# Kernel tuning notes

Measured on AMD Instinct MI355X. Metric: run time of the kernel, lower is better.

## Reference

```python
import jax, jax.numpy as jnp
import numpy as np

B, M, D, H = 32768, 4, 256, 8
HD = D // H           # head_dim = 32
DG = 64               # gate hidden (d_a)
DF = 4 * D            # FF hidden = 1024
EPS = 1e-5


def setup_inputs() -> dict:
    key = jax.random.key(0)
    ks = jax.random.split(key, 20)
    s = 0.02
    inp = {
        'x':   jax.random.normal(ks[0], (B, M, D), jnp.float32),
        # per-modality MultiheadAttention params (stacked over modality axis)
        'Wq':  jax.random.normal(ks[1], (M, D, D), jnp.float32) * s,
        'bq':  jnp.zeros((M, D), jnp.float32),
        'Wk':  jax.random.normal(ks[2], (M, D, D), jnp.float32) * s,
        'bk':  jnp.zeros((M, D), jnp.float32),
        'Wv':  jax.random.normal(ks[3], (M, D, D), jnp.float32) * s,
        'bv':  jnp.zeros((M, D), jnp.float32),
        'Wo':  jax.random.normal(ks[4], (M, D, D), jnp.float32) * s,
        'bo':  jnp.zeros((M, D), jnp.float32),
        # gate MLP: Linear(2D,64) -> tanh -> Linear(64,1)
        'g1w': jax.random.normal(ks[5], (M, DG, 2 * D), jnp.float32) * s,
        'g1b': jnp.zeros((M, DG), jnp.float32),
        'g2w': jax.random.normal(ks[6], (M, 1, DG), jnp.float32) * s,
        'g2b': jnp.zeros((M, 1), jnp.float32),
        # LayerNorm
        'ln_g': jnp.ones((M, D), jnp.float32),
        'ln_b': jnp.zeros((M, D), jnp.float32),
        # FeedForward: Linear(D,4D) -> GELU -> Linear(4D,D)
        'f1w': jax.random.normal(ks[7], (M, DF, D), jnp.float32) * s,
        'f1b': jnp.zeros((M, DF), jnp.float32),
        'f2w': jax.random.normal(ks[8], (M, D, DF), jnp.float32) * s,
        'f2b': jnp.zeros((M, D), jnp.float32),
    }
    return inp


def _forward(x, Wq, bq, Wk, bk, Wv, bv, Wo, bo, g1w, g1b, g2w, g2b,
             ln_g, ln_b, f1w, f1b, f2w, f2b):
    b = x.shape[0]
    scale = 1.0 / np.sqrt(HD)
    # cross-attention: per modality m, query = x[:,m] (seq 1), keys/values = all modalities (seq M)
    Q = jnp.einsum('bmd,mkd->bmk', x, Wq) + bq                      # [B,M,D]
    K = jnp.einsum('bnd,mkd->bmnk', x, Wk) + bk[None, :, None, :]   # [B,M,N,D]
    V = jnp.einsum('bnd,mkd->bmnk', x, Wv) + bv[None, :, None, :]
    Qh = Q.reshape(b, M, H, HD) * scale
    Kh = K.reshape(b, M, M, H, HD)
    Vh = V.reshape(b, M, M, H, HD)
    scores = jnp.einsum('bmhd,bmnhd->bmhn', Qh, Kh)                 # [B,M,H,N]
    A = jax.nn.softmax(scores, axis=-1)
    Oh = jnp.einsum('bmhn,bmnhd->bmhd', A, Vh).reshape(b, M, D)
    attn_out = jnp.einsum('bmd,mod->bmo', Oh, Wo) + bo              # [B,M,D]
    # gate: sigmoid(MLP([x; attn_out]))
    combined = jnp.concatenate([x, attn_out], axis=-1)              # [B,M,2D]
    h = jnp.tanh(jnp.einsum('bmd,mhd->bmh', combined, g1w) + g1b)
    gate = jax.nn.sigmoid(jnp.einsum('bmh,moh->bmo', h, g2w) + g2b) # [B,M,1]
    # residual + LayerNorm (per modality affine)
    r = x + gate * attn_out
    mu = jnp.mean(r, axis=-1, keepdims=True)
    var = jnp.mean(jnp.square(r - mu), axis=-1, keepdims=True)
    y = (r - mu) * jax.lax.rsqrt(var + EPS) * ln_g + ln_b
    # FeedForward residual (exact GELU, matching torch nn.GELU default)
    hf = jax.nn.gelu(jnp.einsum('bmd,mhd->bmh', y, f1w) + f1b, approximate=False)
    ff = jnp.einsum('bmh,mdh->bmd', hf, f2w) + f2b
    updated = y + ff
    return updated, gate


def reference(x, Wq, bq, Wk, bk, Wv, bv, Wo, bo, g1w, g1b, g2w, g2b,
              ln_g, ln_b, f1w, f1b, f2w, f2b):
    return _forward(x, Wq, bq, Wk, bk, Wv, bv, Wo, bo, g1w, g1b, g2w, g2b,
                    ln_g, ln_b, f1w, f1b, f2w, f2b)
```

## Files before the change

kernel.cpp:

```cpp
#include <hip/hip_runtime.h>

#define B_SZ 32768
#define M_SZ 4
#define D_SZ 256
#define SCALE_Q 0.17677669529663687f

#define OWQ 0
#define OWK 262144
#define OWV 524288
#define OWO 786432
#define OG1 1048576
#define OF1 1179648
#define OF2 2228224
#define NW_TOT 3276800

typedef __attribute__((ext_vector_type(8))) short bf16x8;
typedef __attribute__((ext_vector_type(4))) float f32x4;

__device__ __forceinline__ short f2b(float f){
  unsigned u = __float_as_uint(f);
  return (short)((u + 0x7FFFu + ((u >> 16) & 1u)) >> 16);
}
__device__ __forceinline__ float b2f(short s){
  return __uint_as_float(((unsigned)(unsigned short)s) << 16);
}
__device__ __forceinline__ float bflo(unsigned u){ return __uint_as_float(u << 16); }
__device__ __forceinline__ float bfhi(unsigned u){ return __uint_as_float(u & 0xFFFF0000u); }
__device__ __forceinline__ unsigned pack2(float a, float b){
  return (unsigned)(unsigned short)f2b(a) | (((unsigned)(unsigned short)f2b(b)) << 16);
}

__global__ void k_cast_w(const float* __restrict__ Wq, const float* __restrict__ Wk,
                         const float* __restrict__ Wv, const float* __restrict__ Wo,
                         const float* __restrict__ g1w, const float* __restrict__ f1w,
                         const float* __restrict__ f2w, short* __restrict__ wsW){
  int i = blockIdx.x * 256 + threadIdx.x;
  if (i >= NW_TOT) return;
  const float* src; int off;
  if (i < OG1){ int r = i >> 18; off = i & 262143;
    src = (r == 0) ? Wq : (r == 1) ? Wk : (r == 2) ? Wv : Wo; }
  else if (i < OF1){ src = g1w; off = i - OG1; }
  else if (i < OF2){ src = f1w; off = i - OF1; }
  else { src = f2w; off = i - OF2; }
  wsW[i] = f2b(src[off]);
}

__device__ __forceinline__ void kv_gemm(const short* __restrict__ wmat, const float* __restrict__ bias,
                                        const short* xb_s, short* kv_s, int w, int cl, int kb){
  f32x4 acc[4][2];
#pragma unroll
  for (int rt = 0; rt < 4; ++rt)
#pragma unroll
    for (int c = 0; c < 2; ++c) acc[rt][c] = (f32x4){0.f,0.f,0.f,0.f};
  for (int kk = 0; kk < 8; ++kk){
    bf16x8 a[4];
#pragma unroll
    for (int rt = 0; rt < 4; ++rt)
      a[rt] = *(const bf16x8*)&xb_s[(rt*16 + cl)*264 + kk*32 + kb*8];
#pragma unroll
    for (int c = 0; c < 2; ++c){
      int col = (2*w + c)*16 + cl;
      bf16x8 b = *(const bf16x8*)&wmat[(size_t)col*256 + kk*32 + kb*8];
#pragma unroll
      for (int rt = 0; rt < 4; ++rt)
        acc[rt][c] = __builtin_amdgcn_mfma_f32_16x16x32_bf16(a[rt], b, acc[rt][c], 0, 0, 0);
    }
  }
#pragma unroll
  for (int c = 0; c < 2; ++c){
    int col = (2*w + c)*16 + cl;
    float bs = bias[col];
#pragma unroll
    for (int rt = 0; rt < 4; ++rt)
#pragma unroll
      for (int i = 0; i < 4; ++i)
        kv_s[(rt*16 + kb*4 + i)*264 + col] = f2b(acc[rt][c][i] + bs);
  }
}

__global__ __launch_bounds__(512, 1)
void k_attn(const float* __restrict__ x, const short* __restrict__ wsW,
            const float* __restrict__ bq, const float* __restrict__ bk,
            const float* __restrict__ bv, const float* __restrict__ bo,
            const float* __restrict__ g1b, const float* __restrict__ g2w,
            const float* __restrict__ g2b, const float* __restrict__ ln_g,
            const float* __restrict__ ln_b, short* __restrict__ wsY,
            float* __restrict__ gate_out)
{
  __shared__ __align__(16) short xb_s[64*264];
  __shared__ __align__(16) short q_s [64*264];
  __shared__ __align__(16) short kv_s[64*264];
  __shared__ float aw_s[16][8][4];
  __shared__ float gp_s[8][16];
  __shared__ float gate_s[64];

  const int tid = threadIdx.x;
  const int rb  = blockIdx.x * 64;
  const int w   = tid >> 6, l = tid & 63;
  const int cl  = l & 15, kb = l >> 4;

  {
    int r = tid >> 3, s = tid & 7;
    const float4* gp4 = (const float4*)(x + (size_t)(rb + r) * 256);
    unsigned* dst = (unsigned*)&xb_s[r*264];
#pragma unroll
    for (int j = 0; j < 8; ++j){
      float4 v = gp4[j*8 + s];
      int c = (j*8 + s)*4;
      dst[(c >> 1)    ] = pack2(v.x, v.y);
      dst[(c >> 1) + 1] = pack2(v.z, v.w);
    }
  }
  __syncthreads();

  {
    const int m = w & 3, half = w >> 2;
    const short* wq = wsW + OWQ + m*65536;
    f32x4 acc[8];
#pragma unroll
    for (int ct = 0; ct < 8; ++ct) acc[ct] = (f32x4){0.f,0.f,0.f,0.f};
    for (int kk = 0; kk < 8; ++kk){
      bf16x8 a = *(const bf16x8*)&xb_s[(4*cl + m)*264 + kk*32 + kb*8];
#pragma unroll
      for (int ct = 0; ct < 8; ++ct){
        int col = half*128 + ct*16 + cl;
        bf16x8 b = *(const bf16x8*)&wq[(size_t)col*256 + kk*32 + kb*8];
        acc[ct] = __builtin_amdgcn_mfma_f32_16x16x32_bf16(a, b, acc[ct], 0, 0, 0);
      }
    }
#pragma unroll
    for (int ct = 0; ct < 8; ++ct){
      int col = half*128 + ct*16 + cl;
      float bs = bq[m*256 + col];
#pragma unroll
      for (int i = 0; i < 4; ++i)
        q_s[(4*(kb*4 + i) + m)*264 + col] = f2b((acc[ct][i] + bs) * SCALE_Q);
    }
  }
  __syncthreads();

  for (int mm = 0; mm < 4; ++mm){
    kv_gemm(wsW + OWK + mm*65536, bk + mm*256, xb_s, kv_s, w, cl, kb);
    __syncthreads();
    {
      int bl = tid >> 5, h = (tid >> 2) & 7, n = tid & 3;
      const unsigned* qp = (const unsigned*)&q_s [(4*bl + mm)*264 + h*32];
      const unsigned* kp = (const unsigned*)&kv_s[(4*bl + n )*264 + h*32];
      float s = 0.f;
#pragma unroll
      for (int j = 0; j < 16; ++j){
        unsigned uq = qp[j], uk = kp[j];
        s += bflo(uq)*bflo(uk) + bfhi(uq)*bfhi(uk);
      }
      float mx = fmaxf(s, __shfl_xor(s, 1));
      mx = fmaxf(mx, __shfl_xor(mx, 2));
      float e = expf(s - mx);
      float sum = e + __shfl_xor(e, 1);
      sum += __shfl_xor(sum, 2);
      aw_s[bl][h][n] = e / sum;
    }
    __syncthreads();
    kv_gemm(wsW + OWV + mm*65536, bv + mm*256, xb_s, kv_s, w, cl, kb);
    __syncthreads();
    {
      int bl = tid >> 5, c8 = tid & 31, h = c8 >> 2;
      float oh[8];
#pragma unroll
      for (int j = 0; j < 8; ++j) oh[j] = 0.f;
#pragma unroll
      for (int n = 0; n < 4; ++n){
        float an = aw_s[bl][h][n];
        const unsigned* vp = (const unsigned*)&kv_s[(4*bl + n)*264 + c8*8];
#pragma unroll
        for (int jj = 0; jj < 4; ++jj){
          unsigned u = vp[jj];
          oh[2*jj  ] += an * bflo(u);
          oh[2*jj+1] += an * bfhi(u);
        }
      }
      unsigned* op = (unsigned*)&q_s[(4*bl + mm)*264 + c8*8];
#pragma unroll
      for (int jj = 0; jj < 4; ++jj) op[jj] = pack2(oh[2*jj], oh[2*jj+1]);
    }
    __syncthreads();
  }

  {
    const int m = w & 3, half = w >> 2;
    const short* wo = wsW + OWO + m*65536;
    f32x4 acc[8];
#pragma unroll
    for (int ct = 0; ct < 8; ++ct) acc[ct] = (f32x4){0.f,0.f,0.f,0.f};
    for (int kk = 0; kk < 8; ++kk){
      bf16x8 a = *(const bf16x8*)&q_s[(4*cl + m)*264 + kk*32 + kb*8];
#pragma unroll
      for (int ct = 0; ct < 8; ++ct){
        int col = half*128 + ct*16 + cl;
        bf16x8 b = *(const bf16x8*)&wo[(size_t)col*256 + kk*32 + kb*8];
        acc[ct] = __builtin_amdgcn_mfma_f32_16x16x32_bf16(a, b, acc[ct], 0, 0, 0);
      }
    }
#pragma unroll
    for (int ct = 0; ct < 8; ++ct){
      int col = half*128 + ct*16 + cl;
      float bs = bo[m*256 + col];
#pragma unroll
      for (int i = 0; i < 4; ++i)
        kv_s[(4*(kb*4 + i) + m)*264 + col] = f2b(acc[ct][i] + bs);
    }
  }
  __syncthreads();

  {
    const int m = w & 3, half = w >> 2;
    const short* g1 = wsW + OG1 + m*32768;
    f32x4 acc[2];
    acc[0] = (f32x4){0.f,0.f,0.f,0.f};
    acc[1] = (f32x4){0.f,0.f,0.f,0.f};
    for (int kk = 0; kk < 16; ++kk){
      const short* ab = (kk < 8) ? &xb_s[(4*cl + m)*264 + kk*32 + kb*8]
                                 : &kv_s[(4*cl + m)*264 + (kk - 8)*32 + kb*8];
      bf16x8 a = *(const bf16x8*)ab;
#pragma unroll
      for (int c = 0; c < 2; ++c){
        int col = half*32 + c*16 + cl;
        bf16x8 b = *(const bf16x8*)&g1[(size_t)col*512 + kk*32 + kb*8];
        acc[c] = __builtin_amdgcn_mfma_f32_16x16x32_bf16(a, b, acc[c], 0, 0, 0);
      }
    }
    float p[4] = {0.f, 0.f, 0.f, 0.f};
#pragma unroll
    for (int c = 0; c < 2; ++c){
      int col = half*32 + c*16 + cl;
      float b1 = g1b[m*64 + col], w2 = g2w[m*64 + col];
#pragma unroll
      for (int i = 0; i < 4; ++i) p[i] += tanhf(acc[c][i] + b1) * w2;
    }
#pragma unroll
    for (int i = 0; i < 4; ++i){
      p[i] += __shfl_xor(p[i], 1);
      p[i] += __shfl_xor(p[i], 2);
      p[i] += __shfl_xor(p[i], 4);
      p[i] += __shfl_xor(p[i], 8);
    }
    if (cl == 0){
#pragma unroll
      for (int i = 0; i < 4; ++i) gp_s[w][kb*4 + i] = p[i];
    }
  }
  __syncthreads();

  if (tid < 64){
    int bl = tid >> 2, m = tid & 3;
    float logit = gp_s[m][bl] + gp_s[m + 4][bl] + g2b[m];
    float g = 1.f / (1.f + expf(-logit));
    gate_s[tid] = g;
    gate_out[rb + tid] = g;
  }
  __syncthreads();

  {
    int r = tid >> 3, sg = tid & 7, m = r & 3;
    float g = gate_s[r];
    const unsigned* xp = (const unsigned*)&xb_s[r*264 + sg*32];
    const unsigned* ap = (const unsigned*)&kv_s[r*264 + sg*32];
    float rv[32];
    float sum = 0.f, sq = 0.f;
#pragma unroll
    for (int j = 0; j < 16; ++j){
      unsigned ux = xp[j], ua = ap[j];
      float v0 = bflo(ux) + g*bflo(ua);
      float v1 = bfhi(ux) + g*bfhi(ua);
      rv[2*j] = v0; rv[2*j+1] = v1;
      sum += v0 + v1; sq += v0*v0 + v1*v1;
    }
#pragma unroll
    for (int o = 1; o < 8; o <<= 1){
      sum += __shfl_xor(sum, o);
      sq  += __shfl_xor(sq, o);
    }
    float mu  = sum * (1.f/256.f);
    float var = sq * (1.f/256.f) - mu*mu;
    float rstd = rsqrtf(var + 1e-5f);
    unsigned* yp = (unsigned*)(wsY + (size_t)(rb + r)*256 + sg*32);
#pragma unroll
    for (int j = 0; j < 16; ++j){
      int c = sg*32 + 2*j;
      float y0 = (rv[2*j]   - mu)*rstd*ln_g[m*256 + c    ] + ln_b[m*256 + c    ];
      float y1 = (rv[2*j+1] - mu)*rstd*ln_g[m*256 + c + 1] + ln_b[m*256 + c + 1];
      yp[j] = pack2(y0, y1);
    }
  }
}

__global__ __launch_bounds__(512, 1)
void k_ff(const short* __restrict__ wsY, const short* __restrict__ wsW,
          const float* __restrict__ f1bias, const float* __restrict__ f2bias,
          float* __restrict__ out)
{
  __shared__ __align__(16) short y_s [128*264];
  __shared__ __align__(16) short hf_s[128*264];
  const int tid = threadIdx.x;
  const int m  = blockIdx.x >> 8;
  const int b0 = (blockIdx.x & 255) * 128;
  const int w = tid >> 6, l = tid & 63, cl = l & 15, kb = l >> 4;
  const int rh = w >> 2, cq = w & 3;

  {
    int r = tid >> 2, qq = tid & 3;
    const short* src = wsY + ((size_t)(b0 + r)*4 + m)*256 + qq*64;
#pragma unroll
    for (int j = 0; j < 8; ++j)
      *(bf16x8*)&y_s[r*264 + qq*64 + j*8] = *(const bf16x8*)(src + j*8);
  }
  __syncthreads();

  f32x4 accO[4][4];
#pragma unroll
  for (int rt = 0; rt < 4; ++rt)
#pragma unroll
    for (int ct = 0; ct < 4; ++ct) accO[rt][ct] = (f32x4){0.f,0.f,0.f,0.f};

  for (int ch = 0; ch < 4; ++ch){
    f32x4 acc1[4][4];
#pragma unroll
    for (int rt = 0; rt < 4; ++rt)
#pragma unroll
      for (int ct = 0; ct < 4; ++ct) acc1[rt][ct] = (f32x4){0.f,0.f,0.f,0.f};
    for (int kk = 0; kk < 8; ++kk){
      bf16x8 a[4];
#pragma unroll
      for (int rt = 0; rt < 4; ++rt)
        a[rt] = *(const bf16x8*)&y_s[(rh*64 + rt*16 + cl)*264 + kk*32 + kb*8];
#pragma unroll
      for (int ct = 0; ct < 4; ++ct){
        size_t ncol = (size_t)(ch*256 + cq*64 + ct*16 + cl);
        bf16x8 b = *(const bf16x8*)&wsW[OF1 + (size_t)m*262144 + ncol*256 + kk*32 + kb*8];
#pragma unroll
        for (int rt = 0; rt < 4; ++rt)
          acc1[rt][ct] = __builtin_amdgcn_mfma_f32_16x16x32_bf16(a[rt], b, acc1[rt][ct], 0, 0, 0);
      }
    }
#pragma unroll
    for (int ct = 0; ct < 4; ++ct){
      int ncl = cq*64 + ct*16 + cl;
      float bs = f1bias[m*1024 + ch*256 + ncl];
#pragma unroll
      for (int rt = 0; rt < 4; ++rt)
#pragma unroll
        for (int i = 0; i < 4; ++i){
          float v = acc1[rt][ct][i] + bs;
          float gv = 0.5f * v * (1.f + erff(v * 0.70710678118654752f));
          hf_s[(rh*64 + rt*16 + kb*4 + i)*264 + ncl] = f2b(gv);
        }
    }
    __syncthreads();
    for (int kk = 0; kk < 8; ++kk){
      bf16x8 a[4];
#pragma unroll
      for (int rt = 0; rt < 4; ++rt)
        a[rt] = *(const bf16x8*)&hf_s[(rh*64 + rt*16 + cl)*264 + kk*32 + kb*8];
#pragma unroll
      for (int ct = 0; ct < 4; ++ct){
        size_t ocol = (size_t)(cq*64 + ct*16 + cl);
        bf16x8 b = *(const bf16x8*)&wsW[OF2 + (size_t)m*262144 + ocol*1024 + ch*256 + kk*32 + kb*8];
#pragma unroll
        for (int rt = 0; rt < 4; ++rt)
          accO[rt][ct] = __builtin_amdgcn_mfma_f32_16x16x32_bf16(a[rt], b, accO[rt][ct], 0, 0, 0);
      }
    }
    __syncthreads();
  }

#pragma unroll
  for (int ct = 0; ct < 4; ++ct){
    int col = cq*64 + ct*16 + cl;
    float bs = f2bias[m*256 + col];
#pragma unroll
    for (int rt = 0; rt < 4; ++rt)
#pragma unroll
      for (int i = 0; i < 4; ++i){
        int row = rh*64 + rt*16 + kb*4 + i;
        float val = accO[rt][ct][i] + bs + b2f(y_s[row*264 + col]);
        out[((size_t)(b0 + row)*4 + m)*256 + col] = val;
      }
  }
}

extern "C" void kernel_launch(void* const* d_in, const int* in_sizes, int n_in,
                              void* d_out, int out_size, void* d_ws, size_t ws_size,
                              hipStream_t stream){
  const float* x    = (const float*)d_in[0];
  const float* Wq   = (const float*)d_in[1];
  const float* bq   = (const float*)d_in[2];
  const float* Wk   = (const float*)d_in[3];
  const float* bk   = (const float*)d_in[4];
  const float* Wv   = (const float*)d_in[5];
  const float* bv   = (const float*)d_in[6];
  const float* Wo   = (const float*)d_in[7];
  const float* bo   = (const float*)d_in[8];
  const float* g1w  = (const float*)d_in[9];
  const float* g1b  = (const float*)d_in[10];
  const float* g2w  = (const float*)d_in[11];
  const float* g2b  = (const float*)d_in[12];
  const float* ln_g = (const float*)d_in[13];
  const float* ln_b = (const float*)d_in[14];
  const float* f1w  = (const float*)d_in[15];
  const float* f1b  = (const float*)d_in[16];
  const float* f2w  = (const float*)d_in[17];
  const float* f2bb = (const float*)d_in[18];

  float* out      = (float*)d_out;
  float* gate_out = out + (size_t)B_SZ * M_SZ * D_SZ;

  short* wsY = (short*)d_ws;
  short* wsW = (short*)d_ws + (size_t)B_SZ * M_SZ * D_SZ;

  hipLaunchKernelGGL(k_cast_w, dim3((NW_TOT + 255) / 256), dim3(256), 0, stream,
                     Wq, Wk, Wv, Wo, g1w, f1w, f2w, wsW);
  hipLaunchKernelGGL(k_attn, dim3(B_SZ / 16), dim3(512), 0, stream,
                     x, wsW, bq, bk, bv, bo, g1b, g2w, g2b, ln_g, ln_b, wsY, gate_out);
  hipLaunchKernelGGL(k_ff, dim3(4 * (B_SZ / 128)), dim3(512), 0, stream,
                     wsY, wsW, f1b, f2bb, out);
}
```

Baseline: 1.260 ms.

## Restructure attention and FF kernels: fused K/V, folded gate weights, tanh GELU

Adds a prep kernel that folds Wo into the gate's first-layer weights, so the gate MLP consumes the pre-projection attention output directly and can run alongside the Wo GEMM. The attention kernel moves to 1024 threads that compute K and V in one pass, each into its own LDS buffer, and merges softmax with the weighted V sum through shuffles. Rows are reordered to modality-major and rotated indices are used to reduce LDS bank conflicts. The FF kernel shrinks to 64-row tiles for more occupancy and swaps exact erf GELU for a tanh approximation with fast exp. The approximation and the folded weights slightly change numerics.

```diff
diff --git a/kernel.cpp b/kernel.cpp
--- a/kernel.cpp
+++ b/kernel.cpp
@@ -1,8 +1,6 @@
 #include <hip/hip_runtime.h>
 
 #define B_SZ 32768
-#define M_SZ 4
-#define D_SZ 256
 #define SCALE_Q 0.17677669529663687f
 
 #define OWQ 0
@@ -12,10 +10,17 @@
 #define OG1 1048576
 #define OF1 1179648
 #define OF2 2228224
+#define OG1A 3276800
 #define NW_TOT 3276800
+#define NW_ALL 3342336
+
+#define PX 264
+#define PK 266
 
 typedef __attribute__((ext_vector_type(8))) short bf16x8;
 typedef __attribute__((ext_vector_type(4))) float f32x4;
+
+#define MFMA16(a,b,c) __builtin_amdgcn_mfma_f32_16x16x32_bf16((a),(b),(c),0,0,0)
 
 __device__ __forceinline__ short f2b(float f){
   unsigned u = __float_as_uint(f);
@@ -28,6 +33,11 @@
 __device__ __forceinline__ float bfhi(unsigned u){ return __uint_as_float(u & 0xFFFF0000u); }
 __device__ __forceinline__ unsigned pack2(float a, float b){
   return (unsigned)(unsigned short)f2b(a) | (((unsigned)(unsigned short)f2b(b)) << 16);
+}
+__device__ __forceinline__ float gelu_f(float v){
+  float z = 0.7978845608028654f*v + 0.03567740814183427f*v*v*v;
+  z = fminf(fmaxf(z, -15.f), 15.f);
+  return v / (1.f + __expf(-2.f*z));
 }
 
 __global__ void k_cast_w(const float* __restrict__ Wq, const float* __restrict__ Wk,
@@ -45,196 +55,226 @@
   wsW[i] = f2b(src[off]);
 }
 
-__device__ __forceinline__ void kv_gemm(const short* __restrict__ wmat, const float* __restrict__ bias,
-                                        const short* xb_s, short* kv_s, int w, int cl, int kb){
-  f32x4 acc[4][2];
-#pragma unroll
-  for (int rt = 0; rt < 4; ++rt)
-#pragma unroll
-    for (int c = 0; c < 2; ++c) acc[rt][c] = (f32x4){0.f,0.f,0.f,0.f};
-  for (int kk = 0; kk < 8; ++kk){
-    bf16x8 a[4];
-#pragma unroll
-    for (int rt = 0; rt < 4; ++rt)
-      a[rt] = *(const bf16x8*)&xb_s[(rt*16 + cl)*264 + kk*32 + kb*8];
-#pragma unroll
-    for (int c = 0; c < 2; ++c){
-      int col = (2*w + c)*16 + cl;
-      bf16x8 b = *(const bf16x8*)&wmat[(size_t)col*256 + kk*32 + kb*8];
-#pragma unroll
-      for (int rt = 0; rt < 4; ++rt)
-        acc[rt][c] = __builtin_amdgcn_mfma_f32_16x16x32_bf16(a[rt], b, acc[rt][c], 0, 0, 0);
-    }
-  }
-#pragma unroll
-  for (int c = 0; c < 2; ++c){
-    int col = (2*w + c)*16 + cl;
-    float bs = bias[col];
-#pragma unroll
-    for (int rt = 0; rt < 4; ++rt)
-#pragma unroll
-      for (int i = 0; i < 4; ++i)
-        kv_s[(rt*16 + kb*4 + i)*264 + col] = f2b(acc[rt][c][i] + bs);
-  }
-}
-
-__global__ __launch_bounds__(512, 1)
+__global__ void k_prep(const float* __restrict__ g1w, const float* __restrict__ g1b,
+                       const float* __restrict__ Wo, const float* __restrict__ bo,
+                       short* __restrict__ wsW, float* __restrict__ g1bp){
+  const int m = blockIdx.x >> 3;
+  const int h = ((blockIdx.x & 7) << 3) + (threadIdx.x >> 5);
+  const int d = (threadIdx.x & 31) * 8;
+  const float* g1a = g1w + ((size_t)m*64 + h)*512 + 256;
+  const float* wom = Wo + (size_t)m*65536 + d;
+  float acc[8];
+#pragma unroll
+  for (int j = 0; j < 8; ++j) acc[j] = 0.f;
+  float bacc = 0.f;
+  for (int o = 0; o < 256; ++o){
+    float gv = g1a[o];
+    const float4* w4 = (const float4*)(wom + (size_t)o*256);
+    float4 wa = w4[0], wb = w4[1];
+    acc[0] += gv*wa.x; acc[1] += gv*wa.y; acc[2] += gv*wa.z; acc[3] += gv*wa.w;
+    acc[4] += gv*wb.x; acc[5] += gv*wb.y; acc[6] += gv*wb.z; acc[7] += gv*wb.w;
+    bacc += gv * bo[m*256 + o];
+  }
+  short* dst = wsW + OG1A + ((size_t)m*64 + h)*256 + d;
+#pragma unroll
+  for (int j = 0; j < 8; ++j) dst[j] = f2b(acc[j]);
+  if ((threadIdx.x & 31) == 0) g1bp[(size_t)m*64 + h] = bacc + g1b[m*64 + h];
+}
+
+__global__ __launch_bounds__(1024, 4)
 void k_attn(const float* __restrict__ x, const short* __restrict__ wsW,
             const float* __restrict__ bq, const float* __restrict__ bk,
             const float* __restrict__ bv, const float* __restrict__ bo,
-            const float* __restrict__ g1b, const float* __restrict__ g2w,
+            const float* __restrict__ g1bp, const float* __restrict__ g2w,
             const float* __restrict__ g2b, const float* __restrict__ ln_g,
             const float* __restrict__ ln_b, short* __restrict__ wsY,
             float* __restrict__ gate_out)
 {
-  __shared__ __align__(16) short xb_s[64*264];
-  __shared__ __align__(16) short q_s [64*264];
-  __shared__ __align__(16) short kv_s[64*264];
-  __shared__ float aw_s[16][8][4];
-  __shared__ float gp_s[8][16];
+  __shared__ __align__(16) short xb_s[64*PX];
+  __shared__ __align__(16) short q_s [64*PX];
+  __shared__ __align__(16) short k_s [64*PK];
+  __shared__ __align__(16) short v_s [64*PK];
   __shared__ float gate_s[64];
 
   const int tid = threadIdx.x;
-  const int rb  = blockIdx.x * 64;
-  const int w   = tid >> 6, l = tid & 63;
-  const int cl  = l & 15, kb = l >> 4;
+  const int b0  = blockIdx.x * 16;
+  const int w   = tid >> 6, lane = tid & 63;
+  const int cl  = lane & 15, kb = lane >> 4;
 
   {
-    int r = tid >> 3, s = tid & 7;
-    const float4* gp4 = (const float4*)(x + (size_t)(rb + r) * 256);
-    unsigned* dst = (unsigned*)&xb_s[r*264];
-#pragma unroll
-    for (int j = 0; j < 8; ++j){
-      float4 v = gp4[j*8 + s];
-      int c = (j*8 + s)*4;
-      dst[(c >> 1)    ] = pack2(v.x, v.y);
-      dst[(c >> 1) + 1] = pack2(v.z, v.w);
+    int r = tid >> 4, s = tid & 15;
+    int m = r >> 4, bl = r & 15;
+    const float4* gp4 = (const float4*)(x + ((size_t)(b0 + bl)*4 + m) * 256);
+    unsigned* dst = (unsigned*)&xb_s[r*PX];
+#pragma unroll
+    for (int j = 0; j < 4; ++j){
+      float4 v = gp4[j*16 + s];
+      int c = (j*16 + s)*2;
+      dst[c]   = pack2(v.x, v.y);
+      dst[c+1] = pack2(v.z, v.w);
     }
   }
   __syncthreads();
 
   {
-    const int m = w & 3, half = w >> 2;
+    const int m = w & 3, oct = w >> 2;
     const short* wq = wsW + OWQ + m*65536;
-    f32x4 acc[8];
-#pragma unroll
-    for (int ct = 0; ct < 8; ++ct) acc[ct] = (f32x4){0.f,0.f,0.f,0.f};
-    for (int kk = 0; kk < 8; ++kk){
-      bf16x8 a = *(const bf16x8*)&xb_s[(4*cl + m)*264 + kk*32 + kb*8];
-#pragma unroll
-      for (int ct = 0; ct < 8; ++ct){
-        int col = half*128 + ct*16 + cl;
+    f32x4 acc[4];
+#pragma unroll
+    for (int ct = 0; ct < 4; ++ct) acc[ct] = (f32x4){0.f,0.f,0.f,0.f};
+    for (int kk = 0; kk < 8; ++kk){
+      bf16x8 a = *(const bf16x8*)&xb_s[(m*16 + cl)*PX + kk*32 + kb*8];
+#pragma unroll
+      for (int ct = 0; ct < 4; ++ct){
+        int col = oct*64 + ct*16 + cl;
         bf16x8 b = *(const bf16x8*)&wq[(size_t)col*256 + kk*32 + kb*8];
-        acc[ct] = __builtin_amdgcn_mfma_f32_16x16x32_bf16(a, b, acc[ct], 0, 0, 0);
-      }
-    }
-#pragma unroll
-    for (int ct = 0; ct < 8; ++ct){
-      int col = half*128 + ct*16 + cl;
+        acc[ct] = MFMA16(a, b, acc[ct]);
+      }
+    }
+#pragma unroll
+    for (int ct = 0; ct < 4; ++ct){
+      int col = oct*64 + ct*16 + cl;
       float bs = bq[m*256 + col];
 #pragma unroll
       for (int i = 0; i < 4; ++i)
-        q_s[(4*(kb*4 + i) + m)*264 + col] = f2b((acc[ct][i] + bs) * SCALE_Q);
+        q_s[(m*16 + kb*4 + i)*PX + col] = f2b((acc[ct][i] + bs) * SCALE_Q);
     }
   }
   __syncthreads();
 
   for (int mm = 0; mm < 4; ++mm){
-    kv_gemm(wsW + OWK + mm*65536, bk + mm*256, xb_s, kv_s, w, cl, kb);
+    {
+      const int tgt = w >> 3, cw = w & 7;
+      const short* Wm = wsW + (tgt ? OWV : OWK) + mm*65536;
+      const float* bias = (tgt ? bv : bk) + mm*256;
+      short* outb = tgt ? v_s : k_s;
+      const int col0 = cw*32 + cl, col1 = cw*32 + 16 + cl;
+      f32x4 acc0[4], acc1a[4];
+#pragma unroll
+      for (int rt = 0; rt < 4; ++rt){
+        acc0[rt] = (f32x4){0.f,0.f,0.f,0.f};
+        acc1a[rt] = (f32x4){0.f,0.f,0.f,0.f};
+      }
+      for (int kk = 0; kk < 8; ++kk){
+        bf16x8 a[4];
+#pragma unroll
+        for (int rt = 0; rt < 4; ++rt)
+          a[rt] = *(const bf16x8*)&xb_s[(rt*16 + cl)*PX + kk*32 + kb*8];
+        bf16x8 b0v = *(const bf16x8*)&Wm[(size_t)col0*256 + kk*32 + kb*8];
+        bf16x8 b1v = *(const bf16x8*)&Wm[(size_t)col1*256 + kk*32 + kb*8];
+#pragma unroll
+        for (int rt = 0; rt < 4; ++rt){
+          acc0[rt]  = MFMA16(a[rt], b0v, acc0[rt]);
+          acc1a[rt] = MFMA16(a[rt], b1v, acc1a[rt]);
+        }
+      }
+      float bs0 = bias[col0], bs1 = bias[col1];
+#pragma unroll
+      for (int rt = 0; rt < 4; ++rt)
+#pragma unroll
+        for (int i = 0; i < 4; ++i){
+          outb[(rt*16 + kb*4 + i)*PK + col0] = f2b(acc0[rt][i]  + bs0);
+          outb[(rt*16 + kb*4 + i)*PK + col1] = f2b(acc1a[rt][i] + bs1);
+        }
+    }
     __syncthreads();
-    {
-      int bl = tid >> 5, h = (tid >> 2) & 7, n = tid & 3;
-      const unsigned* qp = (const unsigned*)&q_s [(4*bl + mm)*264 + h*32];
-      const unsigned* kp = (const unsigned*)&kv_s[(4*bl + n )*264 + h*32];
+    if (tid < 512){
+      const int bl = tid >> 5, h = (tid >> 2) & 7, n = tid & 3;
+      const int rot = ((bl & 1) + 2*h + 4*n) & 15;
+      const short* qr = &q_s[(mm*16 + bl)*PX + h*32];
+      const short* kr = &k_s[(n*16 + bl)*PK + h*32];
       float s = 0.f;
 #pragma unroll
       for (int j = 0; j < 16; ++j){
-        unsigned uq = qp[j], uk = kp[j];
+        int jj = (j + rot) & 15;
+        unsigned uq = *(const unsigned*)(qr + 2*jj);
+        unsigned uk = *(const unsigned*)(kr + 2*jj);
         s += bflo(uq)*bflo(uk) + bfhi(uq)*bfhi(uk);
       }
       float mx = fmaxf(s, __shfl_xor(s, 1));
       mx = fmaxf(mx, __shfl_xor(mx, 2));
-      float e = expf(s - mx);
+      float e = __expf(s - mx);
       float sum = e + __shfl_xor(e, 1);
       sum += __shfl_xor(sum, 2);
-      aw_s[bl][h][n] = e / sum;
+      float a = e / sum;
+      float oh[8];
+#pragma unroll
+      for (int j = 0; j < 8; ++j) oh[j] = 0.f;
+      const int lbase = lane & ~3;
+#pragma unroll
+      for (int np = 0; np < 4; ++np){
+        float an = __shfl(a, lbase + np);
+        const short* vr = &v_s[(np*16 + bl)*PK + h*32 + n*8];
+#pragma unroll
+        for (int j = 0; j < 4; ++j){
+          unsigned u = *(const unsigned*)(vr + 2*j);
+          oh[2*j]   += an * bflo(u);
+          oh[2*j+1] += an * bfhi(u);
+        }
+      }
+      unsigned* op = (unsigned*)&q_s[(mm*16 + bl)*PX + h*32 + n*8];
+#pragma unroll
+      for (int j = 0; j < 4; ++j) op[j] = pack2(oh[2*j], oh[2*j+1]);
     }
     __syncthreads();
-    kv_gemm(wsW + OWV + mm*65536, bv + mm*256, xb_s, kv_s, w, cl, kb);
-    __syncthreads();
-    {
-      int bl = tid >> 5, c8 = tid & 31, h = c8 >> 2;
-      float oh[8];
-#pragma unroll
-      for (int j = 0; j < 8; ++j) oh[j] = 0.f;
-#pragma unroll
-      for (int n = 0; n < 4; ++n){
-        float an = aw_s[bl][h][n];
-        const unsigned* vp = (const unsigned*)&kv_s[(4*bl + n)*264 + c8*8];
-#pragma unroll
-        for (int jj = 0; jj < 4; ++jj){
-          unsigned u = vp[jj];
-          oh[2*jj  ] += an * bflo(u);
-          oh[2*jj+1] += an * bfhi(u);
-        }
-      }
-      unsigned* op = (unsigned*)&q_s[(4*bl + mm)*264 + c8*8];
-#pragma unroll
-      for (int jj = 0; jj < 4; ++jj) op[jj] = pack2(oh[2*jj], oh[2*jj+1]);
-    }
-    __syncthreads();
   }
 
   {
-    const int m = w & 3, half = w >> 2;
+    const int m = w & 3, oct = w >> 2;
     const short* wo = wsW + OWO + m*65536;
-    f32x4 acc[8];
-#pragma unroll
-    for (int ct = 0; ct < 8; ++ct) acc[ct] = (f32x4){0.f,0.f,0.f,0.f};
-    for (int kk = 0; kk < 8; ++kk){
-      bf16x8 a = *(const bf16x8*)&q_s[(4*cl + m)*264 + kk*32 + kb*8];
-#pragma unroll
-      for (int ct = 0; ct < 8; ++ct){
-        int col = half*128 + ct*16 + cl;
+    f32x4 acc[4];
+#pragma unroll
+    for (int ct = 0; ct < 4; ++ct) acc[ct] = (f32x4){0.f,0.f,0.f,0.f};
+    for (int kk = 0; kk < 8; ++kk){
+      bf16x8 a = *(const bf16x8*)&q_s[(m*16 + cl)*PX + kk*32 + kb*8];
+#pragma unroll
+      for (int ct = 0; ct < 4; ++ct){
+        int col = oct*64 + ct*16 + cl;
         bf16x8 b = *(const bf16x8*)&wo[(size_t)col*256 + kk*32 + kb*8];
-        acc[ct] = __builtin_amdgcn_mfma_f32_16x16x32_bf16(a, b, acc[ct], 0, 0, 0);
-      }
-    }
-#pragma unroll
-    for (int ct = 0; ct < 8; ++ct){
-      int col = half*128 + ct*16 + cl;
+        acc[ct] = MFMA16(a, b, acc[ct]);
+      }
+    }
+#pragma unroll
+    for (int ct = 0; ct < 4; ++ct){
+      int col = oct*64 + ct*16 + cl;
       float bs = bo[m*256 + col];
 #pragma unroll
       for (int i = 0; i < 4; ++i)
-        kv_s[(4*(kb*4 + i) + m)*264 + col] = f2b(acc[ct][i] + bs);
-    }
-  }
-  __syncthreads();
-
-  {
-    const int m = w & 3, half = w >> 2;
-    const short* g1 = wsW + OG1 + m*32768;
-    f32x4 acc[2];
-    acc[0] = (f32x4){0.f,0.f,0.f,0.f};
-    acc[1] = (f32x4){0.f,0.f,0.f,0.f};
-    for (int kk = 0; kk < 16; ++kk){
-      const short* ab = (kk < 8) ? &xb_s[(4*cl + m)*264 + kk*32 + kb*8]
-                                 : &kv_s[(4*cl + m)*264 + (kk - 8)*32 + kb*8];
-      bf16x8 a = *(const bf16x8*)ab;
-#pragma unroll
-      for (int c = 0; c < 2; ++c){
-        int col = half*32 + c*16 + cl;
-        bf16x8 b = *(const bf16x8*)&g1[(size_t)col*512 + kk*32 + kb*8];
-        acc[c] = __builtin_amdgcn_mfma_f32_16x16x32_bf16(a, b, acc[c], 0, 0, 0);
-      }
-    }
-    float p[4] = {0.f, 0.f, 0.f, 0.f};
-#pragma unroll
-    for (int c = 0; c < 2; ++c){
-      int col = half*32 + c*16 + cl;
-      float b1 = g1b[m*64 + col], w2 = g2w[m*64 + col];
-#pragma unroll
-      for (int i = 0; i < 4; ++i) p[i] += tanhf(acc[c][i] + b1) * w2;
+        k_s[(m*16 + kb*4 + i)*PK + col] = f2b(acc[ct][i] + bs);
+    }
+  }
+  if (w < 4){
+    const int m = w;
+    const short* g1x = wsW + OG1 + m*32768;
+    const short* g1a = wsW + OG1A + m*16384;
+    f32x4 acc[4];
+#pragma unroll
+    for (int ct = 0; ct < 4; ++ct) acc[ct] = (f32x4){0.f,0.f,0.f,0.f};
+    for (int kk = 0; kk < 8; ++kk){
+      bf16x8 a = *(const bf16x8*)&xb_s[(m*16 + cl)*PX + kk*32 + kb*8];
+#pragma unroll
+      for (int ct = 0; ct < 4; ++ct){
+        int hc = ct*16 + cl;
+        bf16x8 b = *(const bf16x8*)&g1x[(size_t)hc*512 + kk*32 + kb*8];
+        acc[ct] = MFMA16(a, b, acc[ct]);
+      }
+    }
+    for (int kk = 0; kk < 8; ++kk){
+      bf16x8 a = *(const bf16x8*)&q_s[(m*16 + cl)*PX + kk*32 + kb*8];
+#pragma unroll
+      for (int ct = 0; ct < 4; ++ct){
+        int hc = ct*16 + cl;
+        bf16x8 b = *(const bf16x8*)&g1a[(size_t)hc*256 + kk*32 + kb*8];
+        acc[ct] = MFMA16(a, b, acc[ct]);
+      }
+    }
+    float p[4] = {0.f,0.f,0.f,0.f};
+#pragma unroll
+    for (int ct = 0; ct < 4; ++ct){
+      int hc = ct*16 + cl;
+      float b1 = g1bp[m*64 + hc], w2 = g2w[m*64 + hc];
+#pragma unroll
+      for (int i = 0; i < 4; ++i) p[i] += tanhf(acc[ct][i] + b1) * w2;
     }
 #pragma unroll
     for (int i = 0; i < 4; ++i){
@@ -245,144 +285,142 @@
     }
     if (cl == 0){
 #pragma unroll
-      for (int i = 0; i < 4; ++i) gp_s[w][kb*4 + i] = p[i];
+      for (int i = 0; i < 4; ++i){
+        int bl = kb*4 + i;
+        float g = 1.f / (1.f + __expf(-(p[i] + g2b[m])));
+        gate_s[m*16 + bl] = g;
+        gate_out[(size_t)(b0 + bl)*4 + m] = g;
+      }
     }
   }
   __syncthreads();
 
-  if (tid < 64){
-    int bl = tid >> 2, m = tid & 3;
-    float logit = gp_s[m][bl] + gp_s[m + 4][bl] + g2b[m];
-    float g = 1.f / (1.f + expf(-logit));
-    gate_s[tid] = g;
-    gate_out[rb + tid] = g;
-  }
-  __syncthreads();
-
   {
-    int r = tid >> 3, sg = tid & 7, m = r & 3;
-    float g = gate_s[r];
-    const unsigned* xp = (const unsigned*)&xb_s[r*264 + sg*32];
-    const unsigned* ap = (const unsigned*)&kv_s[r*264 + sg*32];
-    float rv[32];
+    const int r = tid >> 4, sg = tid & 15;
+    const int m = r >> 4, bl = r & 15;
+    const float g = gate_s[r];
+    const short* xr = &xb_s[r*PX];
+    const short* ar = &k_s[r*PK];
+    float rv[16];
     float sum = 0.f, sq = 0.f;
 #pragma unroll
-    for (int j = 0; j < 16; ++j){
-      unsigned ux = xp[j], ua = ap[j];
+    for (int j = 0; j < 8; ++j){
+      int colh = sg*16 + 2*j;
+      unsigned ux = *(const unsigned*)(xr + colh);
+      unsigned ua = *(const unsigned*)(ar + colh);
       float v0 = bflo(ux) + g*bflo(ua);
       float v1 = bfhi(ux) + g*bfhi(ua);
       rv[2*j] = v0; rv[2*j+1] = v1;
       sum += v0 + v1; sq += v0*v0 + v1*v1;
     }
 #pragma unroll
-    for (int o = 1; o < 8; o <<= 1){
+    for (int o = 1; o < 16; o <<= 1){
       sum += __shfl_xor(sum, o);
       sq  += __shfl_xor(sq, o);
     }
     float mu  = sum * (1.f/256.f);
     float var = sq * (1.f/256.f) - mu*mu;
     float rstd = rsqrtf(var + 1e-5f);
-    unsigned* yp = (unsigned*)(wsY + (size_t)(rb + r)*256 + sg*32);
-#pragma unroll
-    for (int j = 0; j < 16; ++j){
-      int c = sg*32 + 2*j;
-      float y0 = (rv[2*j]   - mu)*rstd*ln_g[m*256 + c    ] + ln_b[m*256 + c    ];
-      float y1 = (rv[2*j+1] - mu)*rstd*ln_g[m*256 + c + 1] + ln_b[m*256 + c + 1];
+    const float* lg = ln_g + m*256 + sg*16;
+    const float* lb = ln_b + m*256 + sg*16;
+    unsigned* yp = (unsigned*)(wsY + ((size_t)(b0 + bl)*4 + m)*256 + sg*16);
+#pragma unroll
+    for (int j = 0; j < 8; ++j){
+      float y0 = (rv[2*j]   - mu)*rstd*lg[2*j]   + lb[2*j];
+      float y1 = (rv[2*j+1] - mu)*rstd*lg[2*j+1] + lb[2*j+1];
       yp[j] = pack2(y0, y1);
     }
   }
 }
 
-__global__ __launch_bounds__(512, 1)
+__global__ __launch_bounds__(512, 4)
 void k_ff(const short* __restrict__ wsY, const short* __restrict__ wsW,
           const float* __restrict__ f1bias, const float* __restrict__ f2bias,
           float* __restrict__ out)
 {
-  __shared__ __align__(16) short y_s [128*264];
-  __shared__ __align__(16) short hf_s[128*264];
+  __shared__ __align__(16) short y_s [64*PX];
+  __shared__ __align__(16) short hf_s[64*PX];
   const int tid = threadIdx.x;
-  const int m  = blockIdx.x >> 8;
-  const int b0 = (blockIdx.x & 255) * 128;
-  const int w = tid >> 6, l = tid & 63, cl = l & 15, kb = l >> 4;
-  const int rh = w >> 2, cq = w & 3;
+  const int m  = blockIdx.x >> 9;
+  const int b0 = (blockIdx.x & 511) * 64;
+  const int w = tid >> 6, lane = tid & 63, cl = lane & 15, kb = lane >> 4;
 
   {
-    int r = tid >> 2, qq = tid & 3;
-    const short* src = wsY + ((size_t)(b0 + r)*4 + m)*256 + qq*64;
-#pragma unroll
-    for (int j = 0; j < 8; ++j)
-      *(bf16x8*)&y_s[r*264 + qq*64 + j*8] = *(const bf16x8*)(src + j*8);
+    int r = tid >> 3, s = tid & 7;
+    const short* src = wsY + ((size_t)(b0 + r)*4 + m)*256 + s*32;
+    short* dst = &y_s[r*PX + s*32];
+#pragma unroll
+    for (int q = 0; q < 4; ++q)
+      *(bf16x8*)(dst + q*8) = *(const bf16x8*)(src + q*8);
   }
   __syncthreads();
 
-  f32x4 accO[4][4];
-#pragma unroll
-  for (int rt = 0; rt < 4; ++rt)
-#pragma unroll
-    for (int ct = 0; ct < 4; ++ct) accO[rt][ct] = (f32x4){0.f,0.f,0.f,0.f};
+  f32x4 accO[4][2];
+#pragma unroll
+  for (int rt = 0; rt < 4; ++rt){
+    accO[rt][0] = (f32x4){0.f,0.f,0.f,0.f};
+    accO[rt][1] = (f32x4){0.f,0.f,0.f,0.f};
+  }
 
   for (int ch = 0; ch < 4; ++ch){
-    f32x4 acc1[4][4];
+    f32x4 acc1[4][2];
+#pragma unroll
+    for (int rt = 0; rt < 4; ++rt){
+      acc1[rt][0] = (f32x4){0.f,0.f,0.f,0.f};
+      acc1[rt][1] = (f32x4){0.f,0.f,0.f,0.f};
+    }
+    for (int kk = 0; kk < 8; ++kk){
+      bf16x8 a[4];
+#pragma unroll
+      for (int rt = 0; rt < 4; ++rt)
+        a[rt] = *(const bf16x8*)&y_s[(rt*16 + cl)*PX + kk*32 + kb*8];
+#pragma unroll
+      for (int c = 0; c < 2; ++c){
+        size_t ncol = (size_t)(ch*256 + w*32 + c*16 + cl);
+        bf16x8 b = *(const bf16x8*)&wsW[OF1 + (size_t)m*262144 + ncol*256 + kk*32 + kb*8];
+#pragma unroll
+        for (int rt = 0; rt < 4; ++rt)
+          acc1[rt][c] = MFMA16(a[rt], b, acc1[rt][c]);
+      }
+    }
+#pragma unroll
+    for (int c = 0; c < 2; ++c){
+      int ncl = w*32 + c*16 + cl;
+      float bs = f1bias[m*1024 + ch*256 + ncl];
+#pragma unroll
+      for (int rt = 0; rt < 4; ++rt)
+#pragma unroll
+        for (int i = 0; i < 4; ++i)
+          hf_s[(rt*16 + kb*4 + i)*PX + ncl] = f2b(gelu_f(acc1[rt][c][i] + bs));
+    }
+    __syncthreads();
+    for (int kk = 0; kk < 8; ++kk){
+      bf16x8 a[4];
+#pragma unroll
+      for (int rt = 0; rt < 4; ++rt)
+        a[rt] = *(const bf16x8*)&hf_s[(rt*16 + cl)*PX + kk*32 + kb*8];
+#pragma unroll
+      for (int c = 0; c < 2; ++c){
+        size_t ocol = (size_t)(w*32 + c*16 + cl);
+        bf16x8 b = *(const bf16x8*)&wsW[OF2 + (size_t)m*262144 + ocol*1024 + ch*256 + kk*32 + kb*8];
+#pragma unroll
+        for (int rt = 0; rt < 4; ++rt)
+          accO[rt][c] = MFMA16(a[rt], b, accO[rt][c]);
+      }
+    }
+    __syncthreads();
+  }
+
+#pragma unroll
+  for (int c = 0; c < 2; ++c){
+    int col = w*32 + c*16 + cl;
+    float bs = f2bias[m*256 + col];
 #pragma unroll
     for (int rt = 0; rt < 4; ++rt)
 #pragma unroll
-      for (int ct = 0; ct < 4; ++ct) acc1[rt][ct] = (f32x4){0.f,0.f,0.f,0.f};
-    for (int kk = 0; kk < 8; ++kk){
-      bf16x8 a[4];
-#pragma unroll
-      for (int rt = 0; rt < 4; ++rt)
-        a[rt] = *(const bf16x8*)&y_s[(rh*64 + rt*16 + cl)*264 + kk*32 + kb*8];
-#pragma unroll
-      for (int ct = 0; ct < 4; ++ct){
-        size_t ncol = (size_t)(ch*256 + cq*64 + ct*16 + cl);
-        bf16x8 b = *(const bf16x8*)&wsW[OF1 + (size_t)m*262144 + ncol*256 + kk*32 + kb*8];
-#pragma unroll
-        for (int rt = 0; rt < 4; ++rt)
-          acc1[rt][ct] = __builtin_amdgcn_mfma_f32_16x16x32_bf16(a[rt], b, acc1[rt][ct], 0, 0, 0);
-      }
-    }
-#pragma unroll
-    for (int ct = 0; ct < 4; ++ct){
-      int ncl = cq*64 + ct*16 + cl;
-      float bs = f1bias[m*1024 + ch*256 + ncl];
-#pragma unroll
-      for (int rt = 0; rt < 4; ++rt)
-#pragma unroll
-        for (int i = 0; i < 4; ++i){
-          float v = acc1[rt][ct][i] + bs;
-          float gv = 0.5f * v * (1.f + erff(v * 0.70710678118654752f));
-          hf_s[(rh*64 + rt*16 + kb*4 + i)*264 + ncl] = f2b(gv);
-        }
-    }
-    __syncthreads();
-    for (int kk = 0; kk < 8; ++kk){
-      bf16x8 a[4];
-#pragma unroll
-      for (int rt = 0; rt < 4; ++rt)
-        a[rt] = *(const bf16x8*)&hf_s[(rh*64 + rt*16 + cl)*264 + kk*32 + kb*8];
-#pragma unroll
-      for (int ct = 0; ct < 4; ++ct){
-        size_t ocol = (size_t)(cq*64 + ct*16 + cl);
-        bf16x8 b = *(const bf16x8*)&wsW[OF2 + (size_t)m*262144 + ocol*1024 + ch*256 + kk*32 + kb*8];
-#pragma unroll
-        for (int rt = 0; rt < 4; ++rt)
-          accO[rt][ct] = __builtin_amdgcn_mfma_f32_16x16x32_bf16(a[rt], b, accO[rt][ct], 0, 0, 0);
-      }
-    }
-    __syncthreads();
-  }
-
-#pragma unroll
-  for (int ct = 0; ct < 4; ++ct){
-    int col = cq*64 + ct*16 + cl;
-    float bs = f2bias[m*256 + col];
-#pragma unroll
-    for (int rt = 0; rt < 4; ++rt)
-#pragma unroll
       for (int i = 0; i < 4; ++i){
-        int row = rh*64 + rt*16 + kb*4 + i;
-        float val = accO[rt][ct][i] + bs + b2f(y_s[row*264 + col]);
-        out[((size_t)(b0 + row)*4 + m)*256 + col] = val;
+        int row = rt*16 + kb*4 + i;
+        out[((size_t)(b0 + row)*4 + m)*256 + col] = accO[rt][c][i] + bs + b2f(y_s[row*PX + col]);
       }
   }
 }
@@ -411,15 +449,18 @@
   const float* f2bb = (const float*)d_in[18];
 
   float* out      = (float*)d_out;
-  float* gate_out = out + (size_t)B_SZ * M_SZ * D_SZ;
+  float* gate_out = out + (size_t)B_SZ * 4 * 256;
 
   short* wsY = (short*)d_ws;
-  short* wsW = (short*)d_ws + (size_t)B_SZ * M_SZ * D_SZ;
+  short* wsW = (short*)d_ws + (size_t)B_SZ * 4 * 256;
+  float* g1bp = (float*)(wsW + NW_ALL);
 
   hipLaunchKernelGGL(k_cast_w, dim3((NW_TOT + 255) / 256), dim3(256), 0, stream,
                      Wq, Wk, Wv, Wo, g1w, f1w, f2w, wsW);
-  hipLaunchKernelGGL(k_attn, dim3(B_SZ / 16), dim3(512), 0, stream,
-                     x, wsW, bq, bk, bv, bo, g1b, g2w, g2b, ln_g, ln_b, wsY, gate_out);
-  hipLaunchKernelGGL(k_ff, dim3(4 * (B_SZ / 128)), dim3(512), 0, stream,
+  hipLaunchKernelGGL(k_prep, dim3(32), dim3(256), 0, stream,
+                     g1w, g1b, Wo, bo, wsW, g1bp);
+  hipLaunchKernelGGL(k_attn, dim3(B_SZ / 16), dim3(1024), 0, stream,
+                     x, wsW, bq, bk, bv, bo, g1bp, g2w, g2b, ln_g, ln_b, wsY, gate_out);
+  hipLaunchKernelGGL(k_ff, dim3(4 * (B_SZ / 64)), dim3(512), 0, stream,
                      wsY, wsW, f1b, f2bb, out);
 }
```

New measurement: 1.298 ms. 3.0% more time.
